# Optimization experiments

Hardware: AMD Instinct MI355X
Metric: run time of the kernel (lower is better)

The kernel has to match this reference:

```python
import jax, jax.numpy as jnp
import numpy as np

N, E = 50000, 800000
D_IN, D_H, D_OUT = 128, 128, 64


def setup_inputs() -> dict:
    key = jax.random.key(0)
    ks = jax.random.split(key, 12)
    x = jax.random.normal(ks[0], (N, D_IN), dtype=jnp.float32)
    edge_index = jax.random.randint(ks[1], (2, E), 0, N, dtype=jnp.int64)
    s = 0.05
    return {
        "x": x,
        "edge_index": edge_index,
        # SAGEConv layer 0: in -> hidden. lin_l (neighbor path, with bias), lin_r (root, no bias)
        "Wl0": jax.random.normal(ks[2], (D_H, D_IN), dtype=jnp.float32) * s,
        "bl0": jnp.zeros((D_H,), dtype=jnp.float32),
        "Wr0": jax.random.normal(ks[3], (D_H, D_IN), dtype=jnp.float32) * s,
        # layer 1: hidden -> hidden
        "Wl1": jax.random.normal(ks[4], (D_H, D_H), dtype=jnp.float32) * s,
        "bl1": jnp.zeros((D_H,), dtype=jnp.float32),
        "Wr1": jax.random.normal(ks[5], (D_H, D_H), dtype=jnp.float32) * s,
        # layer 2: hidden -> out
        "Wl2": jax.random.normal(ks[6], (D_OUT, D_H), dtype=jnp.float32) * s,
        "bl2": jnp.zeros((D_OUT,), dtype=jnp.float32),
        "Wr2": jax.random.normal(ks[7], (D_OUT, D_H), dtype=jnp.float32) * s,
    }


def reference(x, edge_index, Wl0, bl0, Wr0, Wl1, bl1, Wr1, Wl2, bl2, Wr2):
    n = x.shape[0]
    src, dst = edge_index[0], edge_index[1]
    # in-degree of each target node (mean aggregation denominator)
    deg = jax.ops.segment_sum(jnp.ones_like(dst, dtype=x.dtype), dst, num_segments=n)
    inv_deg = (1.0 / jnp.maximum(deg, 1.0))[:, None]  # [N,1]; zero-degree -> sum is 0 anyway

    def sage_conv(h, Wl, bl, Wr):
        # mean-aggregate neighbor features: gather h[src], scatter-add to dst
        agg = jax.ops.segment_sum(h[src], dst, num_segments=n) * inv_deg  # [N, d]
        return agg @ Wl.T + bl + h @ Wr.T

    h = jax.nn.relu(sage_conv(x, Wl0, bl0, Wr0))
    # dropout p=0 in eval mode (training=False, force_dropout=False) -> no-op
    h = jax.nn.relu(sage_conv(h, Wl1, bl1, Wr1))
    return sage_conv(h, Wl2, bl2, Wr2)
```

## Files before the change

### kernel.cpp

```cpp
#include <hip/hip_runtime.h>


#define D_H 128
#define NBUCKET 196
#define EPB 8192
#define NBLK 98

typedef _Float16 half8  __attribute__((ext_vector_type(8)));
typedef _Float16 half4v __attribute__((ext_vector_type(4)));
typedef float    floatx4 __attribute__((ext_vector_type(4)));

__global__ __launch_bounds__(256) void hist_convert_kernel(
        const int* __restrict__ dst, int* __restrict__ histo, int E,
        const float* __restrict__ x, _Float16* __restrict__ xh, int n4,
        const float* __restrict__ w0, const float* __restrict__ w1,
        const float* __restrict__ w2, const float* __restrict__ w3,
        const float* __restrict__ w4, const float* __restrict__ w5,
        _Float16* __restrict__ o0, _Float16* __restrict__ o1,
        _Float16* __restrict__ o2, _Float16* __restrict__ o3,
        _Float16* __restrict__ o4, _Float16* __restrict__ o5) {
    if (blockIdx.x < NBLK) {
        __shared__ int h[NBUCKET];
        for (int i = threadIdx.x; i < NBUCKET; i += 256) h[i] = 0;
        __syncthreads();
        int base = blockIdx.x * EPB;
        int end = min(base + EPB, E);
        for (int i = base + threadIdx.x; i < end; i += 256)
            atomicAdd(&h[dst[i] >> 8], 1);
        __syncthreads();
        for (int i = threadIdx.x; i < NBUCKET; i += 256)
            histo[blockIdx.x * NBUCKET + i] = h[i];
        return;
    }
    int i = (blockIdx.x - NBLK) * 256 + threadIdx.x;
    const float* in; _Float16* out; int j;
    if (i < n4) { in = x; out = xh; j = i; }
    else {
        int k = i - n4;
        if      (k <  4096) { in = w0; out = o0; j = k; }
        else if (k <  8192) { in = w1; out = o1; j = k - 4096; }
        else if (k < 12288) { in = w2; out = o2; j = k - 8192; }
        else if (k < 16384) { in = w3; out = o3; j = k - 12288; }
        else if (k < 18432) { in = w4; out = o4; j = k - 16384; }
        else if (k < 20480) { in = w5; out = o5; j = k - 18432; }
        else return;
    }
    float4 v = ((const float4*)in)[j];
    half4v o = { (_Float16)v.x, (_Float16)v.y, (_Float16)v.z, (_Float16)v.w };
    ((half4v*)out)[j] = o;
}

__global__ __launch_bounds__(256) void scan_hist_kernel(const int* __restrict__ histo,
                                                        int* __restrict__ offs,
                                                        int* __restrict__ boff,
                                                        int* __restrict__ row_ptr, int n) {
    __shared__ int s[256];
    int t = threadIdx.x;
    int sum = 0;
    if (t < NBUCKET) {
        for (int b = 0; b < NBLK; ++b) {
            offs[b * NBUCKET + t] = sum;
            sum += histo[b * NBUCKET + t];
        }
    }
    s[t] = (t < NBUCKET) ? sum : 0;
    int tot = s[t];
    __syncthreads();
    for (int off = 1; off < 256; off <<= 1) {
        int tmp = (t >= off) ? s[t - off] : 0;
        __syncthreads();
        s[t] += tmp;
        __syncthreads();
    }
    int base = s[t] - tot;
    if (t < NBUCKET) boff[t] = base;
    if (t == 255) { boff[NBUCKET] = s[255]; row_ptr[n] = s[255]; }
    __syncthreads();
    if (t < NBUCKET)
        for (int b = 0; b < NBLK; ++b)
            offs[b * NBUCKET + t] += base;
}

__global__ __launch_bounds__(256) void scatter_kernel(const int* __restrict__ src,
                                                      const int* __restrict__ dst,
                                                      const int* __restrict__ offs,
                                                      unsigned int* __restrict__ bedge, int E) {
    __shared__ int lcur[NBUCKET];
    for (int i = threadIdx.x; i < NBUCKET; i += 256)
        lcur[i] = offs[blockIdx.x * NBUCKET + i];
    __syncthreads();
    int base = blockIdx.x * EPB;
    int end = min(base + EPB, E);
    for (int i = base + threadIdx.x; i < end; i += 256) {
        int d = dst[i];
        int pos = atomicAdd(&lcur[d >> 8], 1);
        bedge[pos] = ((unsigned int)(d & 255) << 16) | (unsigned int)src[i];
    }
}

__global__ __launch_bounds__(256) void bucket_build_kernel(const unsigned int* __restrict__ bedge,
                                                           const int* __restrict__ boff,
                                                           int* __restrict__ row_ptr,
                                                           float* __restrict__ inv_deg,
                                                           int* __restrict__ col, int n) {
    __shared__ int sdeg[256];
    __shared__ int sscan[256];
    __shared__ int lcur[256];
    const int b = blockIdx.x;
    const int t = threadIdx.x;
    const int base = boff[b];
    const int bend = boff[b + 1];
    sdeg[t] = 0;
    __syncthreads();
    for (int i = base + t; i < bend; i += 256)
        atomicAdd(&sdeg[bedge[i] >> 16], 1);
    __syncthreads();
    int d = sdeg[t];
    sscan[t] = d;
    __syncthreads();
    for (int off = 1; off < 256; off <<= 1) {
        int tmp = (t >= off) ? sscan[t - off] : 0;
        __syncthreads();
        sscan[t] += tmp;
        __syncthreads();
    }
    int excl = sscan[t] - d;
    int node = b * 256 + t;
    if (node < n) {
        row_ptr[node] = base + excl;
        inv_deg[node] = 1.0f / (float)max(d, 1);
    }
    lcur[t] = excl;
    __syncthreads();
    for (int i = base + t; i < bend; i += 256) {
        unsigned int v = bedge[i];
        int pos = atomicAdd(&lcur[v >> 16], 1);
        col[base + pos] = (int)(v & 0xffffu);
    }
}

__global__ __launch_bounds__(128, 8) void aggregate_kernel(const _Float16* __restrict__ h,
                                                           const int* __restrict__ row_ptr,
                                                           const int* __restrict__ col,
                                                           const float* __restrict__ inv_deg,
                                                           _Float16* __restrict__ agg, int n) {
    int wave = threadIdx.x >> 6;
    int lane = threadIdx.x & 63;
    int node = blockIdx.x * 2 + wave;
    if (node >= n) return;
    int beg = row_ptr[node];
    int end = row_ptr[node + 1];
    const int quarter = lane >> 4;
    const int off = (lane & 15) << 3;
    float a0f = 0.f, a1f = 0.f, a2f = 0.f, a3f = 0.f;
    float a4f = 0.f, a5f = 0.f, a6f = 0.f, a7f = 0.f;
    for (int base = beg; base < end; base += 64) {
        int m = end - base;
        if (m > 64) m = 64;
        int myc = (lane < m) ? col[base + lane] : 0;
        int t = 0;
        for (; t + 4 <= (m >> 2); t += 4) {
            int u0 = __shfl(myc, ((t + 0) << 2) + quarter);
            int u1 = __shfl(myc, ((t + 1) << 2) + quarter);
            int u2 = __shfl(myc, ((t + 2) << 2) + quarter);
            int u3 = __shfl(myc, ((t + 3) << 2) + quarter);
            half8 v0 = *(const half8*)&h[(size_t)u0 * D_H + off];
            half8 v1 = *(const half8*)&h[(size_t)u1 * D_H + off];
            half8 v2 = *(const half8*)&h[(size_t)u2 * D_H + off];
            half8 v3 = *(const half8*)&h[(size_t)u3 * D_H + off];
            a0f += (float)v0[0] + (float)v1[0] + (float)v2[0] + (float)v3[0];
            a1f += (float)v0[1] + (float)v1[1] + (float)v2[1] + (float)v3[1];
            a2f += (float)v0[2] + (float)v1[2] + (float)v2[2] + (float)v3[2];
            a3f += (float)v0[3] + (float)v1[3] + (float)v2[3] + (float)v3[3];
            a4f += (float)v0[4] + (float)v1[4] + (float)v2[4] + (float)v3[4];
            a5f += (float)v0[5] + (float)v1[5] + (float)v2[5] + (float)v3[5];
            a6f += (float)v0[6] + (float)v1[6] + (float)v2[6] + (float)v3[6];
            a7f += (float)v0[7] + (float)v1[7] + (float)v2[7] + (float)v3[7];
        }
        int smax = (m + 3) >> 2;
        for (; t < smax; ++t) {
            int j = (t << 2) + quarter;
            int u = __shfl(myc, j);
            if (j < m) {
                half8 v = *(const half8*)&h[(size_t)u * D_H + off];
                a0f += (float)v[0]; a1f += (float)v[1];
                a2f += (float)v[2]; a3f += (float)v[3];
                a4f += (float)v[4]; a5f += (float)v[5];
                a6f += (float)v[6]; a7f += (float)v[7];
            }
        }
    }
    a0f += __shfl(a0f, lane + 16); a1f += __shfl(a1f, lane + 16);
    a2f += __shfl(a2f, lane + 16); a3f += __shfl(a3f, lane + 16);
    a4f += __shfl(a4f, lane + 16); a5f += __shfl(a5f, lane + 16);
    a6f += __shfl(a6f, lane + 16); a7f += __shfl(a7f, lane + 16);
    a0f += __shfl(a0f, lane + 32); a1f += __shfl(a1f, lane + 32);
    a2f += __shfl(a2f, lane + 32); a3f += __shfl(a3f, lane + 32);
    a4f += __shfl(a4f, lane + 32); a5f += __shfl(a5f, lane + 32);
    a6f += __shfl(a6f, lane + 32); a7f += __shfl(a7f, lane + 32);
    if (quarter == 0) {
        float s = inv_deg[node];
        half8 o = { (_Float16)(a0f * s), (_Float16)(a1f * s),
                    (_Float16)(a2f * s), (_Float16)(a3f * s),
                    (_Float16)(a4f * s), (_Float16)(a5f * s),
                    (_Float16)(a6f * s), (_Float16)(a7f * s) };
        *(half8*)&agg[(size_t)node * D_H + off] = o;
    }
}

__global__ __launch_bounds__(128, 8) void aggregate_add64_kernel(
        const _Float16* __restrict__ T,
        const _Float16* __restrict__ Rh,
        const int* __restrict__ row_ptr,
        const int* __restrict__ col,
        const float* __restrict__ inv_deg,
        float* __restrict__ out, int n) {
    int wave = threadIdx.x >> 6;
    int lane = threadIdx.x & 63;
    int node = blockIdx.x * 2 + wave;
    if (node >= n) return;
    int beg = row_ptr[node];
    int end = row_ptr[node + 1];
    const int quarter = lane >> 4;
    const int off = (lane & 15) << 2;
    float a0f = 0.f, a1f = 0.f, a2f = 0.f, a3f = 0.f;
    for (int base = beg; base < end; base += 64) {
        int m = end - base;
        if (m > 64) m = 64;
        int myc = (lane < m) ? col[base + lane] : 0;
        int t = 0;
        for (; t + 4 <= (m >> 2); t += 4) {
            int u0 = __shfl(myc, ((t + 0) << 2) + quarter);
            int u1 = __shfl(myc, ((t + 1) << 2) + quarter);
            int u2 = __shfl(myc, ((t + 2) << 2) + quarter);
            int u3 = __shfl(myc, ((t + 3) << 2) + quarter);
            half4v v0 = *(const half4v*)&T[(size_t)u0 * 64 + off];
            half4v v1 = *(const half4v*)&T[(size_t)u1 * 64 + off];
            half4v v2 = *(const half4v*)&T[(size_t)u2 * 64 + off];
            half4v v3 = *(const half4v*)&T[(size_t)u3 * 64 + off];
            a0f += (float)v0[0] + (float)v1[0] + (float)v2[0] + (float)v3[0];
            a1f += (float)v0[1] + (float)v1[1] + (float)v2[1] + (float)v3[1];
            a2f += (float)v0[2] + (float)v1[2] + (float)v2[2] + (float)v3[2];
            a3f += (float)v0[3] + (float)v1[3] + (float)v2[3] + (float)v3[3];
        }
        int smax = (m + 3) >> 2;
        for (; t < smax; ++t) {
            int j = (t << 2) + quarter;
            int u = __shfl(myc, j);
            if (j < m) {
                half4v v = *(const half4v*)&T[(size_t)u * 64 + off];
                a0f += (float)v[0]; a1f += (float)v[1];
                a2f += (float)v[2]; a3f += (float)v[3];
            }
        }
    }
    a0f += __shfl(a0f, lane + 16); a1f += __shfl(a1f, lane + 16);
    a2f += __shfl(a2f, lane + 16); a3f += __shfl(a3f, lane + 16);
    a0f += __shfl(a0f, lane + 32); a1f += __shfl(a1f, lane + 32);
    a2f += __shfl(a2f, lane + 32); a3f += __shfl(a3f, lane + 32);
    if (quarter == 0) {
        float s = inv_deg[node];
        half4v r = *(const half4v*)&Rh[(size_t)node * 64 + off];
        float4 o;
        o.x = (float)r[0] + a0f * s;
        o.y = (float)r[1] + a1f * s;
        o.z = (float)r[2] + a2f * s;
        o.w = (float)r[3] + a3f * s;
        *(float4*)&out[(size_t)node * 64 + off] = o;
    }
}

template<int NT, bool RELU_HALF_OUT>
__global__ __launch_bounds__(128) void gemm_mfma_kernel(
        const _Float16* __restrict__ Xa, const _Float16* __restrict__ Xh,
        const _Float16* __restrict__ Wa, const _Float16* __restrict__ Wh,
        const float* __restrict__ bias,
        _Float16* __restrict__ out_h, float* __restrict__ out_f, int N) {
    const int wave = threadIdx.x >> 6;
    const int lane = threadIdx.x & 63;
    const int r16 = lane & 15;
    const int quad = lane >> 4;
    const int base = blockIdx.x * 64 + wave * 32;
    const int koff = quad * 8;

    floatx4 acc[2][NT];
    #pragma unroll
    for (int s = 0; s < 2; ++s)
        #pragma unroll
        for (int j = 0; j < NT; ++j)
            acc[s][j] = (floatx4){0.f, 0.f, 0.f, 0.f};

    #pragma unroll
    for (int hsel = 0; hsel < 2; ++hsel) {
        const _Float16* __restrict__ X = hsel ? Xh : Xa;
        const _Float16* __restrict__ W = hsel ? Wh : Wa;
        #pragma unroll
        for (int k0 = 0; k0 < 128; k0 += 32) {
            half8 a0 = *(const half8*)&X[(size_t)(base + r16) * 128 + k0 + koff];
            half8 a1 = *(const half8*)&X[(size_t)(base + 16 + r16) * 128 + k0 + koff];
            #pragma unroll
            for (int j = 0; j < NT; ++j) {
                half8 b = *(const half8*)&W[(size_t)(j * 16 + r16) * 128 + k0 + koff];
                acc[0][j] = __builtin_amdgcn_mfma_f32_16x16x32_f16(a0, b, acc[0][j], 0, 0, 0);
                acc[1][j] = __builtin_amdgcn_mfma_f32_16x16x32_f16(a1, b, acc[1][j], 0, 0, 0);
            }
        }
    }

    #pragma unroll
    for (int s = 0; s < 2; ++s) {
        #pragma unroll
        for (int i = 0; i < 4; ++i) {
            int r = base + s * 16 + quad * 4 + i;
            if (r >= N) continue;
            #pragma unroll
            for (int j = 0; j < NT; ++j) {
                int c = j * 16 + r16;
                float v = acc[s][j][i] + bias[c];
                if (RELU_HALF_OUT) {
                    v = fmaxf(v, 0.f);
                    out_h[(size_t)r * (NT * 16) + c] = (_Float16)v;
                } else {
                    out_f[(size_t)r * (NT * 16) + c] = v;
                }
            }
        }
    }
}

__global__ __launch_bounds__(128) void gemm_dual_kernel(
        const _Float16* __restrict__ B, const _Float16* __restrict__ Wl,
        const _Float16* __restrict__ Wr, const float* __restrict__ bias,
        _Float16* __restrict__ T, _Float16* __restrict__ Rh, int N) {
    const int wave = threadIdx.x >> 6;
    const int lane = threadIdx.x & 63;
    const int r16 = lane & 15;
    const int quad = lane >> 4;
    const int base = blockIdx.x * 64 + wave * 32;
    const int koff = quad * 8;

    floatx4 accT[2][4], accR[2][4];
    #pragma unroll
    for (int s = 0; s < 2; ++s)
        #pragma unroll
        for (int j = 0; j < 4; ++j) {
            accT[s][j] = (floatx4){0.f, 0.f, 0.f, 0.f};
            accR[s][j] = (floatx4){0.f, 0.f, 0.f, 0.f};
        }

    #pragma unroll
    for (int k0 = 0; k0 < 128; k0 += 32) {
        half8 a0 = *(const half8*)&B[(size_t)(base + r16) * 128 + k0 + koff];
        half8 a1 = *(const half8*)&B[(size_t)(base + 16 + r16) * 128 + k0 + koff];
        #pragma unroll
        for (int j = 0; j < 4; ++j) {
            half8 bl = *(const half8*)&Wl[(size_t)(j * 16 + r16) * 128 + k0 + koff];
            half8 br = *(const half8*)&Wr[(size_t)(j * 16 + r16) * 128 + k0 + koff];
            accT[0][j] = __builtin_amdgcn_mfma_f32_16x16x32_f16(a0, bl, accT[0][j], 0, 0, 0);
            accT[1][j] = __builtin_amdgcn_mfma_f32_16x16x32_f16(a1, bl, accT[1][j], 0, 0, 0);
            accR[0][j] = __builtin_amdgcn_mfma_f32_16x16x32_f16(a0, br, accR[0][j], 0, 0, 0);
            accR[1][j] = __builtin_amdgcn_mfma_f32_16x16x32_f16(a1, br, accR[1][j], 0, 0, 0);
        }
    }

    #pragma unroll
    for (int s = 0; s < 2; ++s) {
        #pragma unroll
        for (int i = 0; i < 4; ++i) {
            int r = base + s * 16 + quad * 4 + i;
            if (r >= N) continue;
            #pragma unroll
            for (int j = 0; j < 4; ++j) {
                int c = j * 16 + r16;
                T[(size_t)r * 64 + c]  = (_Float16)accT[s][j][i];
                Rh[(size_t)r * 64 + c] = (_Float16)(accR[s][j][i] + bias[c]);
            }
        }
    }
}

extern "C" void kernel_launch(void* const* d_in, const int* in_sizes, int n_in,
                              void* d_out, int out_size, void* d_ws, size_t ws_size,
                              hipStream_t stream) {
    const float* x   = (const float*)d_in[0];
    const int*   edge = (const int*)d_in[1];
    const float* Wl0 = (const float*)d_in[2];
    const float* bl0 = (const float*)d_in[3];
    const float* Wr0 = (const float*)d_in[4];
    const float* Wl1 = (const float*)d_in[5];
    const float* bl1 = (const float*)d_in[6];
    const float* Wr1 = (const float*)d_in[7];
    const float* Wl2 = (const float*)d_in[8];
    const float* bl2 = (const float*)d_in[9];
    const float* Wr2 = (const float*)d_in[10];
    float* out = (float*)d_out;

    const int N = in_sizes[0] / D_H;
    const int E = in_sizes[1] / 2;
    const int* src = edge;
    const int* dst = edge + E;

    const int gx = (N + 63) / 64;
    const int Np = gx * 64;
    const size_t HBYTES = (size_t)Np * D_H * 2;

    char* w = (char*)d_ws;
    char* P0 = w;  w += HBYTES;
    char* P1 = w;  w += HBYTES;
    char* P2 = w;  w += HBYTES;
    _Float16* Wl0h = (_Float16*)w;  w += (size_t)128 * 128 * 2;
    _Float16* Wr0h = (_Float16*)w;  w += (size_t)128 * 128 * 2;
    _Float16* Wl1h = (_Float16*)w;  w += (size_t)128 * 128 * 2;
    _Float16* Wr1h = (_Float16*)w;  w += (size_t)128 * 128 * 2;
    _Float16* Wl2h = (_Float16*)w;  w += (size_t)64 * 128 * 2;
    _Float16* Wr2h = (_Float16*)w;  w += (size_t)64 * 128 * 2;
    int* row_ptr = (int*)w;      w += (size_t)(N + 16) * 4;
    float* inv_deg = (float*)w;  w += (size_t)N * 4;
    int* col     = (int*)w;      w += (size_t)E * 4;
    int* histo   = (int*)w;      w += (size_t)NBLK * NBUCKET * 4;
    int* offs    = (int*)w;      w += (size_t)NBLK * NBUCKET * 4;
    int* boff    = (int*)w;      w += (size_t)(NBUCKET + 1) * 4;

    _Float16* xh   = (_Float16*)P0;
    _Float16* Bh   = (_Float16*)P0;
    unsigned int* bedge = (unsigned int*)P1;
    _Float16* Ah   = (_Float16*)P1;
    _Float16* aggh = (_Float16*)P2;
    _Float16* T    = (_Float16*)P2;
    _Float16* Rh   = (_Float16*)(P2 + HBYTES / 2);

    const int n4 = N * D_H / 4;
    const int conv_blocks = (n4 + 20480 + 255) / 256;
    hist_convert_kernel<<<NBLK + conv_blocks, 256, 0, stream>>>(
        dst, histo, E, x, xh, n4,
        Wl0, Wr0, Wl1, Wr1, Wl2, Wr2,
        Wl0h, Wr0h, Wl1h, Wr1h, Wl2h, Wr2h);

    scan_hist_kernel<<<1, 256, 0, stream>>>(histo, offs, boff, row_ptr, N);
    scatter_kernel<<<NBLK, 256, 0, stream>>>(src, dst, offs, bedge, E);
    bucket_build_kernel<<<NBUCKET, 256, 0, stream>>>(bedge, boff, row_ptr, inv_deg, col, N);

    const int agg_grid = (N + 1) / 2;

    aggregate_kernel<<<agg_grid, 128, 0, stream>>>(xh, row_ptr, col, inv_deg, aggh, N);
    gemm_mfma_kernel<8, true><<<gx, 128, 0, stream>>>(aggh, xh, Wl0h, Wr0h, bl0, Ah, nullptr, N);

    aggregate_kernel<<<agg_grid, 128, 0, stream>>>(Ah, row_ptr, col, inv_deg, aggh, N);
    gemm_mfma_kernel<8, true><<<gx, 128, 0, stream>>>(aggh, Ah, Wl1h, Wr1h, bl1, Bh, nullptr, N);

    gemm_dual_kernel<<<gx, 128, 0, stream>>>(Bh, Wl2h, Wr2h, bl2, T, Rh, N);
    aggregate_add64_kernel<<<agg_grid, 128, 0, stream>>>(T, Rh, row_ptr, col,
                                                         inv_deg, out, N);
}
```

Before: 293.5 us.

## Transform-then-aggregate for all layers and overlap layer-0 GEMM with CSR build

Layers 0 and 1 now apply the linear projections first (T = h·Wl^T, R = h·Wr^T + bias) and then gather-average T, fusing the residual add and ReLU into the aggregation kernel. The layer-0 GEMM reads the fp32 input directly and is split into tiles that run as extra blocks inside the scan, scatter and bucket-build kernels, so it overlaps the CSR construction. This removes the separate x-to-fp16 conversion pass and the standalone layer-0 GEMM launch. The cost is an extra intermediate R buffer per layer and a separate bedge buffer, plus load-balance risk from the fixed C0/C1 tile split across the fused kernels.

```diff
diff --git a/kernel.cpp b/kernel.cpp
--- a/kernel.cpp
+++ b/kernel.cpp
@@ -10,9 +10,8 @@
 typedef _Float16 half4v __attribute__((ext_vector_type(4)));
 typedef float    floatx4 __attribute__((ext_vector_type(4)));
 
-__global__ __launch_bounds__(256) void hist_convert_kernel(
+__global__ __launch_bounds__(256) void hist_wconv_kernel(
         const int* __restrict__ dst, int* __restrict__ histo, int E,
-        const float* __restrict__ x, _Float16* __restrict__ xh, int n4,
         const float* __restrict__ w0, const float* __restrict__ w1,
         const float* __restrict__ w2, const float* __restrict__ w3,
         const float* __restrict__ w4, const float* __restrict__ w5,
@@ -32,118 +31,212 @@
             histo[blockIdx.x * NBUCKET + i] = h[i];
         return;
     }
-    int i = (blockIdx.x - NBLK) * 256 + threadIdx.x;
+    int k = (blockIdx.x - NBLK) * 256 + threadIdx.x;
     const float* in; _Float16* out; int j;
-    if (i < n4) { in = x; out = xh; j = i; }
-    else {
-        int k = i - n4;
-        if      (k <  4096) { in = w0; out = o0; j = k; }
-        else if (k <  8192) { in = w1; out = o1; j = k - 4096; }
-        else if (k < 12288) { in = w2; out = o2; j = k - 8192; }
-        else if (k < 16384) { in = w3; out = o3; j = k - 12288; }
-        else if (k < 18432) { in = w4; out = o4; j = k - 16384; }
-        else if (k < 20480) { in = w5; out = o5; j = k - 18432; }
-        else return;
-    }
+    if      (k <  4096) { in = w0; out = o0; j = k; }
+    else if (k <  8192) { in = w1; out = o1; j = k - 4096; }
+    else if (k < 12288) { in = w2; out = o2; j = k - 8192; }
+    else if (k < 16384) { in = w3; out = o3; j = k - 12288; }
+    else if (k < 18432) { in = w4; out = o4; j = k - 16384; }
+    else if (k < 20480) { in = w5; out = o5; j = k - 18432; }
+    else return;
     float4 v = ((const float4*)in)[j];
     half4v o = { (_Float16)v.x, (_Float16)v.y, (_Float16)v.z, (_Float16)v.w };
     ((half4v*)out)[j] = o;
 }
 
-__global__ __launch_bounds__(256) void scan_hist_kernel(const int* __restrict__ histo,
-                                                        int* __restrict__ offs,
-                                                        int* __restrict__ boff,
-                                                        int* __restrict__ row_ptr, int n) {
-    __shared__ int s[256];
-    int t = threadIdx.x;
-    int sum = 0;
-    if (t < NBUCKET) {
-        for (int b = 0; b < NBLK; ++b) {
-            offs[b * NBUCKET + t] = sum;
-            sum += histo[b * NBUCKET + t];
-        }
-    }
-    s[t] = (t < NBUCKET) ? sum : 0;
-    int tot = s[t];
-    __syncthreads();
-    for (int off = 1; off < 256; off <<= 1) {
-        int tmp = (t >= off) ? s[t - off] : 0;
-        __syncthreads();
-        s[t] += tmp;
-        __syncthreads();
-    }
-    int base = s[t] - tot;
-    if (t < NBUCKET) boff[t] = base;
-    if (t == 255) { boff[NBUCKET] = s[255]; row_ptr[n] = s[255]; }
-    __syncthreads();
-    if (t < NBUCKET)
-        for (int b = 0; b < NBLK; ++b)
-            offs[b * NBUCKET + t] += base;
-}
-
-__global__ __launch_bounds__(256) void scatter_kernel(const int* __restrict__ src,
-                                                      const int* __restrict__ dst,
-                                                      const int* __restrict__ offs,
-                                                      unsigned int* __restrict__ bedge, int E) {
-    __shared__ int lcur[NBUCKET];
-    for (int i = threadIdx.x; i < NBUCKET; i += 256)
-        lcur[i] = offs[blockIdx.x * NBUCKET + i];
-    __syncthreads();
-    int base = blockIdx.x * EPB;
-    int end = min(base + EPB, E);
-    for (int i = base + threadIdx.x; i < end; i += 256) {
-        int d = dst[i];
-        int pos = atomicAdd(&lcur[d >> 8], 1);
-        bedge[pos] = ((unsigned int)(d & 255) << 16) | (unsigned int)src[i];
-    }
-}
-
-__global__ __launch_bounds__(256) void bucket_build_kernel(const unsigned int* __restrict__ bedge,
-                                                           const int* __restrict__ boff,
-                                                           int* __restrict__ row_ptr,
-                                                           float* __restrict__ inv_deg,
-                                                           int* __restrict__ col, int n) {
-    __shared__ int sdeg[256];
-    __shared__ int sscan[256];
-    __shared__ int lcur[256];
-    const int b = blockIdx.x;
-    const int t = threadIdx.x;
-    const int base = boff[b];
-    const int bend = boff[b + 1];
-    sdeg[t] = 0;
-    __syncthreads();
-    for (int i = base + t; i < bend; i += 256)
-        atomicAdd(&sdeg[bedge[i] >> 16], 1);
-    __syncthreads();
-    int d = sdeg[t];
-    sscan[t] = d;
-    __syncthreads();
-    for (int off = 1; off < 256; off <<= 1) {
-        int tmp = (t >= off) ? sscan[t - off] : 0;
-        __syncthreads();
-        sscan[t] += tmp;
-        __syncthreads();
-    }
-    int excl = sscan[t] - d;
-    int node = b * 256 + t;
-    if (node < n) {
-        row_ptr[node] = base + excl;
-        inv_deg[node] = 1.0f / (float)max(d, 1);
-    }
-    lcur[t] = excl;
-    __syncthreads();
-    for (int i = base + t; i < bend; i += 256) {
-        unsigned int v = bedge[i];
-        int pos = atomicAdd(&lcur[v >> 16], 1);
-        col[base + pos] = (int)(v & 0xffffu);
-    }
-}
-
-__global__ __launch_bounds__(128, 8) void aggregate_kernel(const _Float16* __restrict__ h,
-                                                           const int* __restrict__ row_ptr,
-                                                           const int* __restrict__ col,
-                                                           const float* __restrict__ inv_deg,
-                                                           _Float16* __restrict__ agg, int n) {
+template<bool F32A>
+__device__ __forceinline__ void dual_tile(
+        const float* __restrict__ Af, const _Float16* __restrict__ Ah,
+        const _Float16* __restrict__ Wl, const _Float16* __restrict__ Wr,
+        const float* __restrict__ bias,
+        _Float16* __restrict__ T, _Float16* __restrict__ R,
+        int N, int g) {
+    const int ntile = (N + 63) >> 6;
+    if (g >= 2 * ntile) return;
+    const bool rpass = g >= ntile;
+    const _Float16* __restrict__ W = rpass ? Wr : Wl;
+    _Float16* __restrict__ O = rpass ? R : T;
+    const int tile = rpass ? g - ntile : g;
+    const int lt   = threadIdx.x & 127;
+    const int wave = lt >> 6;
+    const int lane = lt & 63;
+    const int r16  = lane & 15;
+    const int quad = lane >> 4;
+    const int base = tile * 64 + wave * 32;
+    const int koff = quad * 8;
+    const int row0 = min(base + r16,      N - 1);
+    const int row1 = min(base + 16 + r16, N - 1);
+
+    floatx4 acc[2][8];
+    #pragma unroll
+    for (int s = 0; s < 2; ++s)
+        #pragma unroll
+        for (int j = 0; j < 8; ++j)
+            acc[s][j] = (floatx4){0.f, 0.f, 0.f, 0.f};
+
+    #pragma unroll
+    for (int k0 = 0; k0 < 128; k0 += 32) {
+        half8 a0, a1;
+        if (F32A) {
+            float4 p0 = *(const float4*)&Af[(size_t)row0 * 128 + k0 + koff];
+            float4 p1 = *(const float4*)&Af[(size_t)row0 * 128 + k0 + koff + 4];
+            float4 q0 = *(const float4*)&Af[(size_t)row1 * 128 + k0 + koff];
+            float4 q1 = *(const float4*)&Af[(size_t)row1 * 128 + k0 + koff + 4];
+            a0 = (half8){ (_Float16)p0.x, (_Float16)p0.y, (_Float16)p0.z, (_Float16)p0.w,
+                          (_Float16)p1.x, (_Float16)p1.y, (_Float16)p1.z, (_Float16)p1.w };
+            a1 = (half8){ (_Float16)q0.x, (_Float16)q0.y, (_Float16)q0.z, (_Float16)q0.w,
+                          (_Float16)q1.x, (_Float16)q1.y, (_Float16)q1.z, (_Float16)q1.w };
+        } else {
+            a0 = *(const half8*)&Ah[(size_t)row0 * 128 + k0 + koff];
+            a1 = *(const half8*)&Ah[(size_t)row1 * 128 + k0 + koff];
+        }
+        #pragma unroll
+        for (int j = 0; j < 8; ++j) {
+            half8 b = *(const half8*)&W[(size_t)(j * 16 + r16) * 128 + k0 + koff];
+            acc[0][j] = __builtin_amdgcn_mfma_f32_16x16x32_f16(a0, b, acc[0][j], 0, 0, 0);
+            acc[1][j] = __builtin_amdgcn_mfma_f32_16x16x32_f16(a1, b, acc[1][j], 0, 0, 0);
+        }
+    }
+
+    #pragma unroll
+    for (int s = 0; s < 2; ++s)
+        #pragma unroll
+        for (int i = 0; i < 4; ++i) {
+            int r = base + s * 16 + quad * 4 + i;
+            if (r >= N) continue;
+            #pragma unroll
+            for (int j = 0; j < 8; ++j) {
+                int c = j * 16 + r16;
+                float v = acc[s][j][i];
+                if (rpass) v += bias[c];
+                O[(size_t)r * 128 + c] = (_Float16)v;
+            }
+        }
+}
+
+__global__ __launch_bounds__(256) void scan_gemm_kernel(
+        const int* __restrict__ histo, int* __restrict__ offs,
+        int* __restrict__ boff, int* __restrict__ row_ptr, int n,
+        const float* __restrict__ x, const _Float16* __restrict__ Wl,
+        const _Float16* __restrict__ Wr, const float* __restrict__ bias,
+        _Float16* __restrict__ T, _Float16* __restrict__ R, int gofs) {
+    if (blockIdx.x == 0) {
+        __shared__ int s[256];
+        int t = threadIdx.x;
+        int sum = 0;
+        if (t < NBUCKET) {
+            for (int b = 0; b < NBLK; ++b) {
+                offs[b * NBUCKET + t] = sum;
+                sum += histo[b * NBUCKET + t];
+            }
+        }
+        s[t] = (t < NBUCKET) ? sum : 0;
+        int tot = s[t];
+        __syncthreads();
+        for (int off = 1; off < 256; off <<= 1) {
+            int tmp = (t >= off) ? s[t - off] : 0;
+            __syncthreads();
+            s[t] += tmp;
+            __syncthreads();
+        }
+        int base = s[t] - tot;
+        if (t < NBUCKET) boff[t] = base;
+        if (t == 255) { boff[NBUCKET] = s[255]; row_ptr[n] = s[255]; }
+        __syncthreads();
+        if (t < NBUCKET)
+            for (int b = 0; b < NBLK; ++b)
+                offs[b * NBUCKET + t] += base;
+        return;
+    }
+    int g = (blockIdx.x - 1) * 2 + (threadIdx.x >> 7) + gofs;
+    dual_tile<true>(x, nullptr, Wl, Wr, bias, T, R, n, g);
+}
+
+__global__ __launch_bounds__(256) void scatter_gemm_kernel(
+        const int* __restrict__ src, const int* __restrict__ dst,
+        const int* __restrict__ offs, unsigned int* __restrict__ bedge, int E,
+        const float* __restrict__ x, const _Float16* __restrict__ Wl,
+        const _Float16* __restrict__ Wr, const float* __restrict__ bias,
+        _Float16* __restrict__ T, _Float16* __restrict__ R, int N, int gofs) {
+    if (blockIdx.x < NBLK) {
+        __shared__ int lcur[NBUCKET];
+        for (int i = threadIdx.x; i < NBUCKET; i += 256)
+            lcur[i] = offs[blockIdx.x * NBUCKET + i];
+        __syncthreads();
+        int base = blockIdx.x * EPB;
+        int end = min(base + EPB, E);
+        for (int i = base + threadIdx.x; i < end; i += 256) {
+            int d = dst[i];
+            int pos = atomicAdd(&lcur[d >> 8], 1);
+            bedge[pos] = ((unsigned int)(d & 255) << 16) | (unsigned int)src[i];
+        }
+        return;
+    }
+    int g = (blockIdx.x - NBLK) * 2 + (threadIdx.x >> 7) + gofs;
+    dual_tile<true>(x, nullptr, Wl, Wr, bias, T, R, N, g);
+}
+
+__global__ __launch_bounds__(256) void bucket_gemm_kernel(
+        const unsigned int* __restrict__ bedge, const int* __restrict__ boff,
+        int* __restrict__ row_ptr, float* __restrict__ inv_deg,
+        int* __restrict__ col, int n,
+        const float* __restrict__ x, const _Float16* __restrict__ Wl,
+        const _Float16* __restrict__ Wr, const float* __restrict__ bias,
+        _Float16* __restrict__ T, _Float16* __restrict__ R, int gofs) {
+    if (blockIdx.x < NBUCKET) {
+        __shared__ int sdeg[256];
+        __shared__ int sscan[256];
+        __shared__ int lcur[256];
+        const int b = blockIdx.x;
+        const int t = threadIdx.x;
+        const int base = boff[b];
+        const int bend = boff[b + 1];
+        sdeg[t] = 0;
+        __syncthreads();
+        for (int i = base + t; i < bend; i += 256)
+            atomicAdd(&sdeg[bedge[i] >> 16], 1);
+        __syncthreads();
+        int d = sdeg[t];
+        sscan[t] = d;
+        __syncthreads();
+        for (int off = 1; off < 256; off <<= 1) {
+            int tmp = (t >= off) ? sscan[t - off] : 0;
+            __syncthreads();
+            sscan[t] += tmp;
+            __syncthreads();
+        }
+        int excl = sscan[t] - d;
+        int node = b * 256 + t;
+        if (node < n) {
+            row_ptr[node] = base + excl;
+            inv_deg[node] = 1.0f / (float)max(d, 1);
+        }
+        lcur[t] = excl;
+        __syncthreads();
+        for (int i = base + t; i < bend; i += 256) {
+            unsigned int v = bedge[i];
+            int pos = atomicAdd(&lcur[v >> 16], 1);
+            col[base + pos] = (int)(v & 0xffffu);
+        }
+        return;
+    }
+    int g = (blockIdx.x - NBUCKET) * 2 + (threadIdx.x >> 7) + gofs;
+    dual_tile<true>(x, nullptr, Wl, Wr, bias, T, R, n, g);
+}
+
+__global__ __launch_bounds__(256) void dual_fp16_kernel(
+        const _Float16* __restrict__ A, const _Float16* __restrict__ Wl,
+        const _Float16* __restrict__ Wr, const float* __restrict__ bias,
+        _Float16* __restrict__ T, _Float16* __restrict__ R, int N) {
+    int g = blockIdx.x * 2 + (threadIdx.x >> 7);
+    dual_tile<false>(nullptr, A, Wl, Wr, bias, T, R, N, g);
+}
+
+__global__ __launch_bounds__(128, 8) void agg_relu_kernel(
+        const _Float16* __restrict__ T, const _Float16* __restrict__ R,
+        const int* __restrict__ row_ptr, const int* __restrict__ col,
+        const float* __restrict__ inv_deg, _Float16* __restrict__ h, int n) {
     int wave = threadIdx.x >> 6;
     int lane = threadIdx.x & 63;
     int node = blockIdx.x * 2 + wave;
@@ -164,10 +257,10 @@
             int u1 = __shfl(myc, ((t + 1) << 2) + quarter);
             int u2 = __shfl(myc, ((t + 2) << 2) + quarter);
             int u3 = __shfl(myc, ((t + 3) << 2) + quarter);
-            half8 v0 = *(const half8*)&h[(size_t)u0 * D_H + off];
-            half8 v1 = *(const half8*)&h[(size_t)u1 * D_H + off];
-            half8 v2 = *(const half8*)&h[(size_t)u2 * D_H + off];
-            half8 v3 = *(const half8*)&h[(size_t)u3 * D_H + off];
+            half8 v0 = *(const half8*)&T[(size_t)u0 * D_H + off];
+            half8 v1 = *(const half8*)&T[(size_t)u1 * D_H + off];
+            half8 v2 = *(const half8*)&T[(size_t)u2 * D_H + off];
+            half8 v3 = *(const half8*)&T[(size_t)u3 * D_H + off];
             a0f += (float)v0[0] + (float)v1[0] + (float)v2[0] + (float)v3[0];
             a1f += (float)v0[1] + (float)v1[1] + (float)v2[1] + (float)v3[1];
             a2f += (float)v0[2] + (float)v1[2] + (float)v2[2] + (float)v3[2];
@@ -182,7 +275,7 @@
             int j = (t << 2) + quarter;
             int u = __shfl(myc, j);
             if (j < m) {
-                half8 v = *(const half8*)&h[(size_t)u * D_H + off];
+                half8 v = *(const half8*)&T[(size_t)u * D_H + off];
                 a0f += (float)v[0]; a1f += (float)v[1];
                 a2f += (float)v[2]; a3f += (float)v[3];
                 a4f += (float)v[4]; a5f += (float)v[5];
@@ -200,11 +293,16 @@
     a6f += __shfl(a6f, lane + 32); a7f += __shfl(a7f, lane + 32);
     if (quarter == 0) {
         float s = inv_deg[node];
-        half8 o = { (_Float16)(a0f * s), (_Float16)(a1f * s),
-                    (_Float16)(a2f * s), (_Float16)(a3f * s),
-                    (_Float16)(a4f * s), (_Float16)(a5f * s),
-                    (_Float16)(a6f * s), (_Float16)(a7f * s) };
-        *(half8*)&agg[(size_t)node * D_H + off] = o;
+        half8 r = *(const half8*)&R[(size_t)node * D_H + off];
+        half8 o = { (_Float16)fmaxf((float)r[0] + a0f * s, 0.f),
+                    (_Float16)fmaxf((float)r[1] + a1f * s, 0.f),
+                    (_Float16)fmaxf((float)r[2] + a2f * s, 0.f),
+                    (_Float16)fmaxf((float)r[3] + a3f * s, 0.f),
+                    (_Float16)fmaxf((float)r[4] + a4f * s, 0.f),
+                    (_Float16)fmaxf((float)r[5] + a5f * s, 0.f),
+                    (_Float16)fmaxf((float)r[6] + a6f * s, 0.f),
+                    (_Float16)fmaxf((float)r[7] + a7f * s, 0.f) };
+        *(half8*)&h[(size_t)node * D_H + off] = o;
     }
 }
 
@@ -270,64 +368,6 @@
     }
 }
 
-template<int NT, bool RELU_HALF_OUT>
-__global__ __launch_bounds__(128) void gemm_mfma_kernel(
-        const _Float16* __restrict__ Xa, const _Float16* __restrict__ Xh,
-        const _Float16* __restrict__ Wa, const _Float16* __restrict__ Wh,
-        const float* __restrict__ bias,
-        _Float16* __restrict__ out_h, float* __restrict__ out_f, int N) {
-    const int wave = threadIdx.x >> 6;
-    const int lane = threadIdx.x & 63;
-    const int r16 = lane & 15;
-    const int quad = lane >> 4;
-    const int base = blockIdx.x * 64 + wave * 32;
-    const int koff = quad * 8;
-
-    floatx4 acc[2][NT];
-    #pragma unroll
-    for (int s = 0; s < 2; ++s)
-        #pragma unroll
-        for (int j = 0; j < NT; ++j)
-            acc[s][j] = (floatx4){0.f, 0.f, 0.f, 0.f};
-
-    #pragma unroll
-    for (int hsel = 0; hsel < 2; ++hsel) {
-        const _Float16* __restrict__ X = hsel ? Xh : Xa;
-        const _Float16* __restrict__ W = hsel ? Wh : Wa;
-        #pragma unroll
-        for (int k0 = 0; k0 < 128; k0 += 32) {
-            half8 a0 = *(const half8*)&X[(size_t)(base + r16) * 128 + k0 + koff];
-            half8 a1 = *(const half8*)&X[(size_t)(base + 16 + r16) * 128 + k0 + koff];
-            #pragma unroll
-            for (int j = 0; j < NT; ++j) {
-                half8 b = *(const half8*)&W[(size_t)(j * 16 + r16) * 128 + k0 + koff];
-                acc[0][j] = __builtin_amdgcn_mfma_f32_16x16x32_f16(a0, b, acc[0][j], 0, 0, 0);
-                acc[1][j] = __builtin_amdgcn_mfma_f32_16x16x32_f16(a1, b, acc[1][j], 0, 0, 0);
-            }
-        }
-    }
-
-    #pragma unroll
-    for (int s = 0; s < 2; ++s) {
-        #pragma unroll
-        for (int i = 0; i < 4; ++i) {
-            int r = base + s * 16 + quad * 4 + i;
-            if (r >= N) continue;
-            #pragma unroll
-            for (int j = 0; j < NT; ++j) {
-                int c = j * 16 + r16;
-                float v = acc[s][j][i] + bias[c];
-                if (RELU_HALF_OUT) {
-                    v = fmaxf(v, 0.f);
-                    out_h[(size_t)r * (NT * 16) + c] = (_Float16)v;
-                } else {
-                    out_f[(size_t)r * (NT * 16) + c] = v;
-                }
-            }
-        }
-    }
-}
-
 __global__ __launch_bounds__(128) void gemm_dual_kernel(
         const _Float16* __restrict__ B, const _Float16* __restrict__ Wl,
         const _Float16* __restrict__ Wr, const float* __restrict__ bias,
@@ -405,9 +445,9 @@
     const size_t HBYTES = (size_t)Np * D_H * 2;
 
     char* w = (char*)d_ws;
-    char* P0 = w;  w += HBYTES;
-    char* P1 = w;  w += HBYTES;
-    char* P2 = w;  w += HBYTES;
+    _Float16* Tb = (_Float16*)w;  w += HBYTES;
+    _Float16* Rb = (_Float16*)w;  w += HBYTES;
+    _Float16* Hb = (_Float16*)w;  w += HBYTES;
     _Float16* Wl0h = (_Float16*)w;  w += (size_t)128 * 128 * 2;
     _Float16* Wr0h = (_Float16*)w;  w += (size_t)128 * 128 * 2;
     _Float16* Wl1h = (_Float16*)w;  w += (size_t)128 * 128 * 2;
@@ -420,35 +460,32 @@
     int* histo   = (int*)w;      w += (size_t)NBLK * NBUCKET * 4;
     int* offs    = (int*)w;      w += (size_t)NBLK * NBUCKET * 4;
     int* boff    = (int*)w;      w += (size_t)(NBUCKET + 1) * 4;
-
-    _Float16* xh   = (_Float16*)P0;
-    _Float16* Bh   = (_Float16*)P0;
-    unsigned int* bedge = (unsigned int*)P1;
-    _Float16* Ah   = (_Float16*)P1;
-    _Float16* aggh = (_Float16*)P2;
-    _Float16* T    = (_Float16*)P2;
-    _Float16* Rh   = (_Float16*)(P2 + HBYTES / 2);
-
-    const int n4 = N * D_H / 4;
-    const int conv_blocks = (n4 + 20480 + 255) / 256;
-    hist_convert_kernel<<<NBLK + conv_blocks, 256, 0, stream>>>(
-        dst, histo, E, x, xh, n4,
+    unsigned int* bedge = (unsigned int*)w;  w += (size_t)E * 4;
+
+    hist_wconv_kernel<<<NBLK + 80, 256, 0, stream>>>(
+        dst, histo, E,
         Wl0, Wr0, Wl1, Wr1, Wl2, Wr2,
         Wl0h, Wr0h, Wl1h, Wr1h, Wl2h, Wr2h);
 
-    scan_hist_kernel<<<1, 256, 0, stream>>>(histo, offs, boff, row_ptr, N);
-    scatter_kernel<<<NBLK, 256, 0, stream>>>(src, dst, offs, bedge, E);
-    bucket_build_kernel<<<NBUCKET, 256, 0, stream>>>(bedge, boff, row_ptr, inv_deg, col, N);
+    const int C0 = 260, C1 = 260, C2 = gx - C0 - C1;
+    scan_gemm_kernel<<<1 + C0, 256, 0, stream>>>(
+        histo, offs, boff, row_ptr, N,
+        x, Wl0h, Wr0h, bl0, Tb, Rb, 0);
+    scatter_gemm_kernel<<<NBLK + C1, 256, 0, stream>>>(
+        src, dst, offs, bedge, E,
+        x, Wl0h, Wr0h, bl0, Tb, Rb, N, 2 * C0);
+    bucket_gemm_kernel<<<NBUCKET + C2, 256, 0, stream>>>(
+        bedge, boff, row_ptr, inv_deg, col, N,
+        x, Wl0h, Wr0h, bl0, Tb, Rb, 2 * (C0 + C1));
 
     const int agg_grid = (N + 1) / 2;
 
-    aggregate_kernel<<<agg_grid, 128, 0, stream>>>(xh, row_ptr, col, inv_deg, aggh, N);
-    gemm_mfma_kernel<8, true><<<gx, 128, 0, stream>>>(aggh, xh, Wl0h, Wr0h, bl0, Ah, nullptr, N);
-
-    aggregate_kernel<<<agg_grid, 128, 0, stream>>>(Ah, row_ptr, col, inv_deg, aggh, N);
-    gemm_mfma_kernel<8, true><<<gx, 128, 0, stream>>>(aggh, Ah, Wl1h, Wr1h, bl1, Bh, nullptr, N);
-
-    gemm_dual_kernel<<<gx, 128, 0, stream>>>(Bh, Wl2h, Wr2h, bl2, T, Rh, N);
-    aggregate_add64_kernel<<<agg_grid, 128, 0, stream>>>(T, Rh, row_ptr, col,
+    agg_relu_kernel<<<agg_grid, 128, 0, stream>>>(Tb, Rb, row_ptr, col, inv_deg, Hb, N);
+
+    dual_fp16_kernel<<<gx, 256, 0, stream>>>(Hb, Wl1h, Wr1h, bl1, Tb, Rb, N);
+    agg_relu_kernel<<<agg_grid, 128, 0, stream>>>(Tb, Rb, row_ptr, col, inv_deg, Hb, N);
+
+    gemm_dual_kernel<<<gx, 128, 0, stream>>>(Hb, Wl2h, Wr2h, bl2, Tb, Rb, N);
+    aggregate_add64_kernel<<<agg_grid, 128, 0, stream>>>(Tb, Rb, row_ptr, col,
                                                          inv_deg, out, N);
 }
```

Result: no change. 298.9 us (+1.8%).
